# Optimization experiments

Hardware: AMD Instinct MI355X
Metric: run time of the kernel (lower is better)

The kernel has to match this reference:

```python
import jax, jax.numpy as jnp
import numpy as np

B, S, E, H = 2, 2048, 768, 12
DK = E // H


def setup_inputs() -> dict:
    key = jax.random.key(0)
    ks = jax.random.split(key, 8)
    scale = 1.0 / np.sqrt(E)
    return {
        "key": jax.random.normal(ks[0], (B, S, E), jnp.float32),
        "query": jax.random.normal(ks[1], (B, S, E), jnp.float32),
        "value": jax.random.normal(ks[2], (B, S, E), jnp.float32),
        "mask": jax.random.randint(ks[3], (1, 1, S, S), 0, 2, jnp.int32),
        # nn.Linear params (w_k used for q/k/v as in the source; w_o output proj)
        "Wk": jax.random.uniform(ks[4], (E, E), jnp.float32, -scale, scale),
        "bk": jax.random.uniform(ks[5], (E,), jnp.float32, -scale, scale),
        "Wo": jax.random.uniform(ks[6], (E, E), jnp.float32, -scale, scale),
        "bo": jax.random.uniform(ks[7], (E,), jnp.float32, -scale, scale),
    }


def reference(key, query, value, mask, Wk, bk, Wo, bo):
    # NOTE: source module (faithfully) projects q, k, v all with w_k.
    k = (key @ Wk.T + bk).reshape(B, S, H, DK).transpose(0, 2, 1, 3)    # [B,H,S,DK]
    q = (query @ Wk.T + bk).reshape(B, S, H, DK).transpose(0, 2, 1, 3)
    v = (value @ Wk.T + bk).reshape(B, S, H, DK).transpose(0, 2, 1, 3)
    # quirk: scores MULTIPLIED by sqrt(d_k) (source bug, preserved)
    scores = jnp.einsum("bhsd,bhtd->bhst", q, k) * jnp.sqrt(jnp.float32(DK))
    # quirk: masked positions set to 1e-6 (not -inf), BEFORE softmax
    scores = jnp.where(mask == 0, jnp.float32(1e-6), scores)
    # dropout=0.0 -> identity (applied pre-softmax in source)
    attn = jax.nn.softmax(scores, axis=-1)                               # [B,H,S,S]
    x = jnp.einsum("bhst,bhtd->bhsd", attn, v)                           # [B,H,S,DK]
    x = x.transpose(0, 2, 1, 3).reshape(B, S, E)
    return x @ Wo.T + bo
```

## Files before the change

kernel.cpp:

```cpp
#include <hip/hip_runtime.h>

#define BB 2
#define SS 2048
#define EE 768
#define HH 12
#define DKK 64

typedef _Float16 h16;
typedef _Float16 half8 __attribute__((ext_vector_type(8)));
typedef _Float16 h16x4 __attribute__((ext_vector_type(4)));
typedef __fp16 pk2 __attribute__((ext_vector_type(2)));
typedef float f32x4 __attribute__((ext_vector_type(4)));

#define K2F 11.5416173f

__device__ __forceinline__ void gl_lds16(const void* g, void* l) {
    __builtin_amdgcn_global_load_lds(
        (const __attribute__((address_space(1))) unsigned int*)g,
        (__attribute__((address_space(3))) unsigned int*)l, 16, 0, 0);
}

__global__ void cvtpack_k(const float* __restrict__ sK, const float* __restrict__ sQ,
                          const float* __restrict__ sV, const float* __restrict__ sWk,
                          const float* __restrict__ sWo,
                          h16* __restrict__ dK, h16* __restrict__ dQ, h16* __restrict__ dV,
                          h16* __restrict__ dWk, h16* __restrict__ dWo,
                          const int* __restrict__ mask, unsigned* __restrict__ mp) {
    if (blockIdx.x >= 5184) {
        int idx = (blockIdx.x - 5184) * 256 + threadIdx.x;
        int base = idx * 32;
        const int4* m4 = (const int4*)(mask + base);
        unsigned w = 0;
#pragma unroll
        for (int i = 0; i < 8; ++i) {
            int4 v = m4[i];
            if (v.x) w |= 1u << (i * 4 + 0);
            if (v.y) w |= 1u << (i * 4 + 1);
            if (v.z) w |= 1u << (i * 4 + 2);
            if (v.w) w |= 1u << (i * 4 + 3);
        }
        mp[idx] = w;
        return;
    }
    long g = (long)blockIdx.x * 256 + threadIdx.x;
    const float* src;
    h16* dst;
    long off;
    if (g < 393216)        { src = sK;  dst = dK;  off = g; }
    else if (g < 786432)   { src = sQ;  dst = dQ;  off = g - 393216; }
    else if (g < 1179648)  { src = sV;  dst = dV;  off = g - 786432; }
    else if (g < 1253376)  { src = sWk; dst = dWk; off = g - 1179648; }
    else                   { src = sWo; dst = dWo; off = g - 1253376; }
    const float* p = src + off * 8;
    float4 a = *(const float4*)p, b = *(const float4*)(p + 4);
    half8 h = {(h16)a.x, (h16)a.y, (h16)a.z, (h16)a.w,
               (h16)b.x, (h16)b.y, (h16)b.z, (h16)b.w};
    *(half8*)(dst + off * 8) = h;
}

__launch_bounds__(256)
__global__ void proj_gemm_k(const h16* __restrict__ keyh, const h16* __restrict__ qryh,
                            const h16* __restrict__ valh, const h16* __restrict__ Wkh,
                            const float* __restrict__ bk,
                            h16* __restrict__ kh, h16* __restrict__ qh, h16* __restrict__ vtp) {
    __shared__ h16 As[64 * 64];
    __shared__ h16 Bs[128 * 64];
    const int bid = blockIdx.x;
    const int idx = (bid & 7) * 144 + (bid >> 3);
    const int z = idx / 384;
    const int rem = idx % 384;
    const int m0 = (rem / 6) * 64, n0 = (rem % 6) * 128;
    const h16* src = (z == 0) ? keyh : ((z == 1) ? qryh : valh);
    const int tid = threadIdx.x, lane = tid & 63, wid = tid >> 6;
    const int l = lane & 15, gq = lane >> 4;
    f32x4 acc[4][2] = {};

    for (int k0 = 0; k0 < EE; k0 += 64) {
#pragma unroll
        for (int it = 0; it < 2; ++it) {
            int e = it * 256 + tid;
            int row = e >> 3, slot = e & 7;
            gl_lds16(src + (long)(m0 + row) * EE + k0 + ((slot ^ (row & 7)) << 3), As + e * 8);
        }
#pragma unroll
        for (int it = 0; it < 4; ++it) {
            int e = it * 256 + tid;
            int row = e >> 3, slot = e & 7;
            gl_lds16(Wkh + (long)(n0 + row) * EE + k0 + ((slot ^ (row & 7)) << 3), Bs + e * 8);
        }
        __syncthreads();
#pragma unroll
        for (int ks = 0; ks < 2; ++ks) {
            half8 a[4], b[2];
#pragma unroll
            for (int rf = 0; rf < 4; ++rf) {
                int row = rf * 16 + l;
                int g = (ks * 4 + gq) ^ (row & 7);
                a[rf] = *(const half8*)((const char*)As + row * 128 + (g << 4));
            }
#pragma unroll
            for (int cf = 0; cf < 2; ++cf) {
                int row = wid * 32 + cf * 16 + l;
                int g = (ks * 4 + gq) ^ (row & 7);
                b[cf] = *(const half8*)((const char*)Bs + row * 128 + (g << 4));
            }
            __builtin_amdgcn_s_setprio(1);
#pragma unroll
            for (int rf = 0; rf < 4; ++rf)
#pragma unroll
                for (int cf = 0; cf < 2; ++cf)
                    acc[rf][cf] = __builtin_amdgcn_mfma_f32_16x16x32_f16(a[rf], b[cf], acc[rf][cf], 0, 0, 0);
            __builtin_amdgcn_s_setprio(0);
        }
        __syncthreads();
    }
    if (z == 2) {
#pragma unroll
        for (int rf = 0; rf < 4; ++rf)
#pragma unroll
            for (int cf = 0; cf < 2; ++cf) {
                int n = n0 + wid * 32 + cf * 16 + l;
                float bias = bk[n];
                int h = n >> 6, d = n & 63;
                int mb = m0 + rf * 16 + gq * 4;
                int b = mb >> 11, s = mb & 2047;
                h16x4 pv = {(h16)(acc[rf][cf][0] + bias), (h16)(acc[rf][cf][1] + bias),
                            (h16)(acc[rf][cf][2] + bias), (h16)(acc[rf][cf][3] + bias)};
                *(h16x4*)(vtp + ((long)((b * HH + h) * 64 + d)) * SS + s) = pv;
            }
    } else {
        h16* dst = (z == 0) ? kh : qh;
        const float qs = (z == 1) ? K2F : 1.0f;
#pragma unroll
        for (int rf = 0; rf < 4; ++rf)
#pragma unroll
            for (int cf = 0; cf < 2; ++cf) {
                int n = n0 + wid * 32 + cf * 16 + l;
                float bias = bk[n];
                int h = n >> 6, d = n & 63;
#pragma unroll
                for (int j = 0; j < 4; ++j) {
                    int m = m0 + rf * 16 + gq * 4 + j;
                    int b = m >> 11, s = m & 2047;
                    dst[(((long)(b * HH + h) * SS + s) << 6) + d] = (h16)((acc[rf][cf][j] + bias) * qs);
                }
            }
    }
}

#define SMX_GROUP(S, MW, M2, LS, PB)                                               \
  {                                                                                \
    unsigned long long mw = (MW);                                                  \
    unsigned w0 = (unsigned)mw, w1 = (unsigned)(mw >> 32);                         \
    _Pragma("unroll")                                                              \
    for (int cf = 0; cf < 4; ++cf) {                                               \
      unsigned wcb = (cf & 2) ? w1 : w0;                                           \
      _Pragma("unroll")                                                            \
      for (int j = 0; j < 4; ++j) {                                                \
        unsigned sh = ((cf & 1) << 4) + g * 4 + j;                                 \
        S[cf][j] = ((wcb >> sh) & 1u) ? S[cf][j] : C2;                             \
      }                                                                            \
    }                                                                              \
    float pmax = fmaxf(fmaxf(S[0][0], S[0][1]), fmaxf(S[0][2], S[0][3]));          \
    _Pragma("unroll")                                                              \
    for (int cf = 1; cf < 4; ++cf)                                                 \
      pmax = fmaxf(pmax, fmaxf(fmaxf(S[cf][0], S[cf][1]), fmaxf(S[cf][2], S[cf][3]))); \
    if (!__all(pmax <= (M2) + 11.0f)) {                                            \
      pmax = fmaxf(pmax, __shfl_xor(pmax, 16));                                    \
      pmax = fmaxf(pmax, __shfl_xor(pmax, 32));                                    \
      float mnew = fmaxf((M2), pmax);                                              \
      float alpha = __builtin_amdgcn_exp2f((M2) - mnew);                           \
      _Pragma("unroll")                                                            \
      for (int df = 0; df < 4; ++df)                                               \
        _Pragma("unroll")                                                          \
        for (int j = 0; j < 4; ++j) o##PB[df][j] *= alpha;                         \
      (LS) *= alpha;                                                               \
      (M2) = mnew;                                                                 \
    }                                                                              \
    const float negm2 = -(M2);                                                     \
    float rs = 0.f;                                                                \
    _Pragma("unroll")                                                              \
    for (int cf = 0; cf < 4; ++cf)                                                 \
      _Pragma("unroll")                                                            \
      for (int j = 0; j < 4; ++j) {                                                \
        float p = __builtin_amdgcn_exp2f(S[cf][j] + negm2);                        \
        S[cf][j] = p;                                                              \
        rs += p;                                                                   \
      }                                                                            \
    (LS) += rs;                                                                    \
    _Pragma("unroll")                                                              \
    for (int cf = 0; cf < 4; ++cf) {                                               \
      union { pk2 h[2]; unsigned long long u; } pu;                                \
      pu.h[0] = __builtin_amdgcn_cvt_pkrtz(S[cf][0], S[cf][1]);                    \
      pu.h[1] = __builtin_amdgcn_cvt_pkrtz(S[cf][2], S[cf][3]);                    \
      *(unsigned long long*)(pb##PB + pst[cf]) = pu.u;                             \
    }                                                                              \
  }

#define ATTN_TILE(KL, VL, KN, VN, T)                                               \
  {                                                                                \
    long nko = (long)((((T) + 1) & 15)) * (64 * DKK);                              \
    int nvo = (((T) + 1) & 15) * 64;                                               \
    gl_lds16(kgl0 + nko, (KN) + stg0);                                             \
    gl_lds16(kgl1 + nko, (KN) + stg1);                                             \
    gl_lds16(vgl0 + nvo, (VN) + stg0);                                             \
    gl_lds16(vgl1 + nvo, (VN) + stg1);                                             \
    half8 ka[4], kb[4];                                                            \
    _Pragma("unroll")                                                              \
    for (int cf = 0; cf < 4; ++cf) {                                               \
      ka[cf] = *(const half8*)((const char*)(KL) + off0 + cf * 2048);              \
      kb[cf] = *(const half8*)((const char*)(KL) + off1 + cf * 2048);              \
    }                                                                              \
    f32x4 sA[4], sB[4];                                                            \
    __builtin_amdgcn_s_setprio(1);                                                 \
    _Pragma("unroll")                                                              \
    for (int cf = 0; cf < 4; ++cf) {                                               \
      f32x4 z = {};                                                                \
      z = __builtin_amdgcn_mfma_f32_16x16x32_f16(ka[cf], qfA0, z, 0, 0, 0);        \
      z = __builtin_amdgcn_mfma_f32_16x16x32_f16(kb[cf], qfA1, z, 0, 0, 0);        \
      sA[cf] = z;                                                                  \
    }                                                                              \
    _Pragma("unroll")                                                              \
    for (int cf = 0; cf < 4; ++cf) {                                               \
      f32x4 z = {};                                                                \
      z = __builtin_amdgcn_mfma_f32_16x16x32_f16(ka[cf], qfB0, z, 0, 0, 0);        \
      z = __builtin_amdgcn_mfma_f32_16x16x32_f16(kb[cf], qfB1, z, 0, 0, 0);        \
      sB[cf] = z;                                                                  \
    }                                                                              \
    __builtin_amdgcn_s_setprio(0);                                                 \
    SMX_GROUP(sA, mrA[T], m2A, lsA, A)                                             \
    SMX_GROUP(sB, mrB[T], m2B, lsB, B)                                             \
    _Pragma("unroll")                                                              \
    for (int ks = 0; ks < 2; ++ks) {                                               \
      int fo = ks ? off1 : off0;                                                   \
      half8 vk[4];                                                                 \
      _Pragma("unroll")                                                            \
      for (int df = 0; df < 4; ++df)                                               \
        vk[df] = *(const half8*)((const char*)(VL) + fo + df * 2048);              \
      half8 pfA = *(const half8*)(pbA + fo);                                       \
      half8 pfB = *(const half8*)(pbB + fo);                                       \
      __builtin_amdgcn_s_setprio(1);                                               \
      _Pragma("unroll")                                                            \
      for (int df = 0; df < 4; ++df)                                               \
        oA[df] = __builtin_amdgcn_mfma_f32_16x16x32_f16(vk[df], pfA, oA[df], 0, 0, 0); \
      _Pragma("unroll")                                                            \
      for (int df = 0; df < 4; ++df)                                               \
        oB[df] = __builtin_amdgcn_mfma_f32_16x16x32_f16(vk[df], pfB, oB[df], 0, 0, 0); \
      __builtin_amdgcn_s_setprio(0);                                               \
    }                                                                              \
    __syncthreads();                                                               \
  }

__launch_bounds__(256, 3)
__global__ void attn_k(const h16* __restrict__ qh, const h16* __restrict__ kh,
                       const h16* __restrict__ vt, const unsigned long long* __restrict__ mp,
                       h16* __restrict__ pO, float* __restrict__ pML) {
    __shared__ h16 K0[4096], K1[4096], V0[4096], V1[4096];
    __shared__ char Ps[16384];
    const int tid = threadIdx.x;
    const int lane = tid & 63, wid = tid >> 6;
    const int l = lane & 15, g = lane >> 4;
    const int bid = blockIdx.x;
    const int idx = (bid & 7) * 96 + (bid >> 3);
    const int bh = idx >> 5;
    const int rem = idx & 31;
    const int qb = rem >> 1, kvh = rem & 1;
    const int q0w = qb * 128 + wid * 32;
    const long base = (long)bh * SS * DKK;
    char* pbA = Ps + wid * 4096;
    char* pbB = pbA + 2048;

    const int off0 = l * 128 + ((g ^ (l & 7)) << 4);
    const int off1 = l * 128 + (((4 + g) ^ (l & 7)) << 4);
    int pst[4];
#pragma unroll
    for (int cf = 0; cf < 4; ++cf)
        pst[cf] = l * 128 + (((2 * cf + (g >> 1)) ^ (l & 7)) << 4) + (g & 1) * 8;
    const int rr = lane >> 3, sg = (lane & 7) ^ (lane >> 3);
    const int stg0 = wid * 1024 + lane * 8, stg1 = wid * 1024 + 512 + lane * 8;
    const int kvbase = kvh * 1024;
    const h16* kgl0 = kh + base + (long)(kvbase + wid * 16 + rr) * DKK + sg * 8;
    const h16* kgl1 = kgl0 + 8 * DKK;
    const h16* vgl0 = vt + base + (long)(wid * 16 + rr) * SS + kvbase + sg * 8;
    const h16* vgl1 = vgl0 + 8 * SS;

    half8 qfA0, qfA1, qfB0, qfB1;
    {
        const h16* qp = qh + base + (long)(q0w + l) * DKK + g * 8;
        qfA0 = *(const half8*)qp;
        qfA1 = *(const half8*)(qp + 32);
        qfB0 = *(const half8*)(qp + 16 * DKK);
        qfB1 = *(const half8*)(qp + 16 * DKK + 32);
    }
    const unsigned long long* mrA = mp + (long)(q0w + l) * (SS / 64) + kvh * 16;
    const unsigned long long* mrB = mrA + 16 * (SS / 64);

    f32x4 oA[4] = {}, oB[4] = {};
    float m2A = -INFINITY, lsA = 0.f, m2B = -INFINITY, lsB = 0.f;
    const float C2 = 1e-6f * 1.44269504f;

    gl_lds16(kgl0, K0 + stg0);
    gl_lds16(kgl1, K0 + stg1);
    gl_lds16(vgl0, V0 + stg0);
    gl_lds16(vgl1, V0 + stg1);
    __syncthreads();

    for (int it = 0; it < 8; ++it) {
        int t = 2 * it;
        ATTN_TILE(K0, V0, K1, V1, t)
        ATTN_TILE(K1, V1, K0, V0, t + 1)
    }

    lsA += __shfl_xor(lsA, 16);
    lsA += __shfl_xor(lsA, 32);
    lsB += __shfl_xor(lsB, 16);
    lsB += __shfl_xor(lsB, 32);
    long prow = ((long)(bh * 2 + kvh) * 2048 + q0w + l);
    h16* pa = pO + (prow << 6) + g * 4;
    h16* pb = pO + ((prow + 16) << 6) + g * 4;
#pragma unroll
    for (int df = 0; df < 4; ++df) {
        h16x4 vA = {(h16)oA[df][0], (h16)oA[df][1], (h16)oA[df][2], (h16)oA[df][3]};
        h16x4 vB = {(h16)oB[df][0], (h16)oB[df][1], (h16)oB[df][2], (h16)oB[df][3]};
        *(h16x4*)(pa + df * 16) = vA;
        *(h16x4*)(pb + df * 16) = vB;
    }
    if (g == 0) {
        float2* mlp = (float2*)(pML + prow * 2);
        *mlp = make_float2(m2A, lsA);
        *(float2*)(pML + (prow + 16) * 2) = make_float2(m2B, lsB);
    }
}

__global__ void combine_k(const h16* __restrict__ pO, const float* __restrict__ pML,
                          h16* __restrict__ xh) {
    int idx = blockIdx.x * 256 + threadIdx.x;
    int d8 = idx & 7;
    int q = (idx >> 3) & 2047;
    int bh = idx >> 14;
    long r0 = (long)(bh * 2) * 2048 + q, r1 = r0 + 2048;
    float2 ml0 = *(const float2*)(pML + r0 * 2);
    float2 ml1 = *(const float2*)(pML + r1 * 2);
    float ms = fmaxf(ml0.x, ml1.x);
    float w0 = __builtin_amdgcn_exp2f(ml0.x - ms);
    float w1 = __builtin_amdgcn_exp2f(ml1.x - ms);
    float inv = 1.0f / (ml0.y * w0 + ml1.y * w1);
    float s0 = w0 * inv, s1 = w1 * inv;
    half8 o0 = *(const half8*)(pO + (r0 << 6) + d8 * 8);
    half8 o1 = *(const half8*)(pO + (r1 << 6) + d8 * 8);
    int b = bh / HH, h = bh % HH;
    half8 r;
#pragma unroll
    for (int i = 0; i < 8; ++i)
        r[i] = (h16)((float)o0[i] * s0 + (float)o1[i] * s1);
    *(half8*)(xh + (long)(b * SS + q) * EE + h * 64 + d8 * 8) = r;
}

__launch_bounds__(256)
__global__ void out_gemm_k(const h16* __restrict__ xh, const h16* __restrict__ Woh,
                           const float* __restrict__ bo, float* __restrict__ out) {
    __shared__ h16 As[64 * 64];
    __shared__ h16 Bs[64 * 64];
    const int bid = blockIdx.x;
    const int idx = (bid & 7) * 96 + (bid >> 3);
    const int m0 = (idx / 12) * 64, n0 = (idx % 12) * 64;
    const int tid = threadIdx.x, lane = tid & 63, wid = tid >> 6;
    const int l = lane & 15, gq = lane >> 4;
    const int wr = wid >> 1, wc = wid & 1;
    f32x4 acc[2][2] = {};

    for (int k0 = 0; k0 < EE; k0 += 64) {
#pragma unroll
        for (int it = 0; it < 2; ++it) {
            int e = it * 256 + tid;
            int row = e >> 3, slot = e & 7;
            int gsl = (slot ^ (row & 7)) << 3;
            gl_lds16(xh + (long)(m0 + row) * EE + k0 + gsl, As + e * 8);
            gl_lds16(Woh + (long)(n0 + row) * EE + k0 + gsl, Bs + e * 8);
        }
        __syncthreads();
#pragma unroll
        for (int ks = 0; ks < 2; ++ks) {
            half8 a[2], b[2];
#pragma unroll
            for (int rf = 0; rf < 2; ++rf) {
                int row = wr * 32 + rf * 16 + l;
                int g = (ks * 4 + gq) ^ (row & 7);
                a[rf] = *(const half8*)((const char*)As + row * 128 + (g << 4));
            }
#pragma unroll
            for (int cf = 0; cf < 2; ++cf) {
                int row = wc * 32 + cf * 16 + l;
                int g = (ks * 4 + gq) ^ (row & 7);
                b[cf] = *(const half8*)((const char*)Bs + row * 128 + (g << 4));
            }
            __builtin_amdgcn_s_setprio(1);
#pragma unroll
            for (int rf = 0; rf < 2; ++rf)
#pragma unroll
                for (int cf = 0; cf < 2; ++cf)
                    acc[rf][cf] = __builtin_amdgcn_mfma_f32_16x16x32_f16(a[rf], b[cf], acc[rf][cf], 0, 0, 0);
            __builtin_amdgcn_s_setprio(0);
        }
        __syncthreads();
    }
#pragma unroll
    for (int rf = 0; rf < 2; ++rf)
#pragma unroll
        for (int cf = 0; cf < 2; ++cf) {
            int n = n0 + wc * 32 + cf * 16 + l;
            float bias = bo[n];
#pragma unroll
            for (int j = 0; j < 4; ++j) {
                int m = m0 + wr * 32 + rf * 16 + gq * 4 + j;
                out[(long)m * EE + n] = acc[rf][cf][j] + bias;
            }
        }
}

extern "C" void kernel_launch(void* const* d_in, const int* in_sizes, int n_in,
                              void* d_out, int out_size, void* d_ws, size_t ws_size,
                              hipStream_t stream) {
    const float* key   = (const float*)d_in[0];
    const float* query = (const float*)d_in[1];
    const float* value = (const float*)d_in[2];
    const int*   mask  = (const int*)d_in[3];
    const float* Wk    = (const float*)d_in[4];
    const float* bk    = (const float*)d_in[5];
    const float* Wo    = (const float*)d_in[6];
    const float* bo    = (const float*)d_in[7];

    char* ws = (char*)d_ws;
    h16* keyh = (h16*)(ws + 0);
    h16* qryh = (h16*)(ws + 6291456);
    h16* valh = (h16*)(ws + 12582912);
    h16* qh   = (h16*)(ws + 18874368);
    h16* kh   = (h16*)(ws + 25165824);
    h16* vt   = (h16*)(ws + 31457280);
    h16* Wkh  = (h16*)(ws + 37748736);
    h16* Woh  = (h16*)(ws + 38928384);
    unsigned* mp = (unsigned*)(ws + 40108032);
    h16*  pO  = (h16*)(ws + 0);
    float* pML = (float*)(ws + 12582912);
    h16*  xh  = (h16*)(ws + 18874368);
    float* out = (float*)d_out;

    hipLaunchKernelGGL(cvtpack_k, dim3(5696), dim3(256), 0, stream,
                       key, query, value, Wk, Wo, keyh, qryh, valh, Wkh, Woh, mask, mp);
    hipLaunchKernelGGL(proj_gemm_k, dim3(1152), dim3(256), 0, stream,
                       keyh, qryh, valh, Wkh, bk, kh, qh, vt);
    hipLaunchKernelGGL(attn_k, dim3(768), dim3(256), 0, stream,
                       qh, kh, vt, (const unsigned long long*)mp, pO, pML);
    hipLaunchKernelGGL(combine_k, dim3(1536), dim3(256), 0, stream, pO, pML, xh);
    hipLaunchKernelGGL(out_gemm_k, dim3(768), dim3(256), 0, stream, xh, Woh, bo, out);
}
```

Before: 115.9 us.

## Split attention KV range three ways and halve P scratch for higher occupancy

```diff
diff --git a/kernel.cpp b/kernel.cpp
--- a/kernel.cpp
+++ b/kernel.cpp
@@ -148,7 +148,7 @@
     }
 }
 
-#define SMX_GROUP(S, MW, M2, LS, PB)                                               \
+#define SMX_GROUP(S, MW, M2, LS, OACC)                                             \
   {                                                                                \
     unsigned long long mw = (MW);                                                  \
     unsigned w0 = (unsigned)mw, w1 = (unsigned)(mw >> 32);                         \
@@ -173,7 +173,7 @@
       _Pragma("unroll")                                                            \
       for (int df = 0; df < 4; ++df)                                               \
         _Pragma("unroll")                                                          \
-        for (int j = 0; j < 4; ++j) o##PB[df][j] *= alpha;                         \
+        for (int j = 0; j < 4; ++j) OACC[df][j] *= alpha;                          \
       (LS) *= alpha;                                                               \
       (M2) = mnew;                                                                 \
     }                                                                              \
@@ -193,14 +193,34 @@
       union { pk2 h[2]; unsigned long long u; } pu;                                \
       pu.h[0] = __builtin_amdgcn_cvt_pkrtz(S[cf][0], S[cf][1]);                    \
       pu.h[1] = __builtin_amdgcn_cvt_pkrtz(S[cf][2], S[cf][3]);                    \
-      *(unsigned long long*)(pb##PB + pst[cf]) = pu.u;                             \
+      *(unsigned long long*)(pb + pst[cf]) = pu.u;                                 \
+    }                                                                              \
+  }
+
+#define PV_GROUP(VL, OACC)                                                         \
+  {                                                                                \
+    _Pragma("unroll")                                                              \
+    for (int ks = 0; ks < 2; ++ks) {                                               \
+      int fo = ks ? off1 : off0;                                                   \
+      half8 pf = *(const half8*)(pb + fo);                                         \
+      half8 vk[4];                                                                 \
+      _Pragma("unroll")                                                            \
+      for (int df = 0; df < 4; ++df)                                               \
+        vk[df] = *(const half8*)((const char*)(VL) + fo + df * 2048);              \
+      __builtin_amdgcn_s_setprio(1);                                               \
+      _Pragma("unroll")                                                            \
+      for (int df = 0; df < 4; ++df)                                               \
+        OACC[df] = __builtin_amdgcn_mfma_f32_16x16x32_f16(vk[df], pf, OACC[df], 0, 0, 0); \
+      __builtin_amdgcn_s_setprio(0);                                               \
     }                                                                              \
   }
 
 #define ATTN_TILE(KL, VL, KN, VN, T)                                               \
   {                                                                                \
-    long nko = (long)((((T) + 1) & 15)) * (64 * DKK);                              \
-    int nvo = (((T) + 1) & 15) * 64;                                               \
+    int tn = (T) + 1;                                                              \
+    if (tn == nt) tn = 0;                                                          \
+    long nko = (long)tn * (64 * DKK);                                              \
+    int nvo = tn * 64;                                                             \
     gl_lds16(kgl0 + nko, (KN) + stg0);                                             \
     gl_lds16(kgl1 + nko, (KN) + stg1);                                             \
     gl_lds16(vgl0 + nvo, (VN) + stg0);                                             \
@@ -228,47 +248,32 @@
       sB[cf] = z;                                                                  \
     }                                                                              \
     __builtin_amdgcn_s_setprio(0);                                                 \
-    SMX_GROUP(sA, mrA[T], m2A, lsA, A)                                             \
-    SMX_GROUP(sB, mrB[T], m2B, lsB, B)                                             \
-    _Pragma("unroll")                                                              \
-    for (int ks = 0; ks < 2; ++ks) {                                               \
-      int fo = ks ? off1 : off0;                                                   \
-      half8 vk[4];                                                                 \
-      _Pragma("unroll")                                                            \
-      for (int df = 0; df < 4; ++df)                                               \
-        vk[df] = *(const half8*)((const char*)(VL) + fo + df * 2048);              \
-      half8 pfA = *(const half8*)(pbA + fo);                                       \
-      half8 pfB = *(const half8*)(pbB + fo);                                       \
-      __builtin_amdgcn_s_setprio(1);                                               \
-      _Pragma("unroll")                                                            \
-      for (int df = 0; df < 4; ++df)                                               \
-        oA[df] = __builtin_amdgcn_mfma_f32_16x16x32_f16(vk[df], pfA, oA[df], 0, 0, 0); \
-      _Pragma("unroll")                                                            \
-      for (int df = 0; df < 4; ++df)                                               \
-        oB[df] = __builtin_amdgcn_mfma_f32_16x16x32_f16(vk[df], pfB, oB[df], 0, 0, 0); \
-      __builtin_amdgcn_s_setprio(0);                                               \
-    }                                                                              \
+    SMX_GROUP(sA, mrA[T], m2A, lsA, oA)                                            \
+    PV_GROUP(VL, oA)                                                               \
+    SMX_GROUP(sB, mrB[T], m2B, lsB, oB)                                            \
+    PV_GROUP(VL, oB)                                                               \
     __syncthreads();                                                               \
   }
 
-__launch_bounds__(256, 3)
+__launch_bounds__(256, 4)
 __global__ void attn_k(const h16* __restrict__ qh, const h16* __restrict__ kh,
                        const h16* __restrict__ vt, const unsigned long long* __restrict__ mp,
                        h16* __restrict__ pO, float* __restrict__ pML) {
     __shared__ h16 K0[4096], K1[4096], V0[4096], V1[4096];
-    __shared__ char Ps[16384];
+    __shared__ char Ps[8192];
     const int tid = threadIdx.x;
     const int lane = tid & 63, wid = tid >> 6;
     const int l = lane & 15, g = lane >> 4;
     const int bid = blockIdx.x;
-    const int idx = (bid & 7) * 96 + (bid >> 3);
-    const int bh = idx >> 5;
-    const int rem = idx & 31;
-    const int qb = rem >> 1, kvh = rem & 1;
+    const int idx = (bid & 7) * 144 + (bid >> 3);
+    const int bh = idx / 48;
+    const int rem = idx % 48;
+    const int qb = rem / 3, kvh = rem % 3;
+    const int nt = (kvh == 2) ? 10 : 11;
+    const int kvt0 = kvh * 11;
     const int q0w = qb * 128 + wid * 32;
     const long base = (long)bh * SS * DKK;
-    char* pbA = Ps + wid * 4096;
-    char* pbB = pbA + 2048;
+    char* pb = Ps + wid * 2048;
 
     const int off0 = l * 128 + ((g ^ (l & 7)) << 4);
     const int off1 = l * 128 + (((4 + g) ^ (l & 7)) << 4);
@@ -278,10 +283,9 @@
         pst[cf] = l * 128 + (((2 * cf + (g >> 1)) ^ (l & 7)) << 4) + (g & 1) * 8;
     const int rr = lane >> 3, sg = (lane & 7) ^ (lane >> 3);
     const int stg0 = wid * 1024 + lane * 8, stg1 = wid * 1024 + 512 + lane * 8;
-    const int kvbase = kvh * 1024;
-    const h16* kgl0 = kh + base + (long)(kvbase + wid * 16 + rr) * DKK + sg * 8;
+    const h16* kgl0 = kh + base + (long)(kvt0 * 64 + wid * 16 + rr) * DKK + sg * 8;
     const h16* kgl1 = kgl0 + 8 * DKK;
-    const h16* vgl0 = vt + base + (long)(wid * 16 + rr) * SS + kvbase + sg * 8;
+    const h16* vgl0 = vt + base + (long)(wid * 16 + rr) * SS + kvt0 * 64 + sg * 8;
     const h16* vgl1 = vgl0 + 8 * SS;
 
     half8 qfA0, qfA1, qfB0, qfB1;
@@ -292,7 +296,7 @@
         qfB0 = *(const half8*)(qp + 16 * DKK);
         qfB1 = *(const half8*)(qp + 16 * DKK + 32);
     }
-    const unsigned long long* mrA = mp + (long)(q0w + l) * (SS / 64) + kvh * 16;
+    const unsigned long long* mrA = mp + (long)(q0w + l) * (SS / 64) + kvt0;
     const unsigned long long* mrB = mrA + 16 * (SS / 64);
 
     f32x4 oA[4] = {}, oB[4] = {};
@@ -305,29 +309,32 @@
     gl_lds16(vgl1, V0 + stg1);
     __syncthreads();
 
-    for (int it = 0; it < 8; ++it) {
+    for (int it = 0; it < (nt >> 1); ++it) {
         int t = 2 * it;
         ATTN_TILE(K0, V0, K1, V1, t)
         ATTN_TILE(K1, V1, K0, V0, t + 1)
+    }
+    if (nt & 1) {
+        int t = nt - 1;
+        ATTN_TILE(K0, V0, K1, V1, t)
     }
 
     lsA += __shfl_xor(lsA, 16);
     lsA += __shfl_xor(lsA, 32);
     lsB += __shfl_xor(lsB, 16);
     lsB += __shfl_xor(lsB, 32);
-    long prow = ((long)(bh * 2 + kvh) * 2048 + q0w + l);
+    long prow = ((long)(bh * 3 + kvh) * 2048 + q0w + l);
     h16* pa = pO + (prow << 6) + g * 4;
-    h16* pb = pO + ((prow + 16) << 6) + g * 4;
+    h16* pbo = pO + ((prow + 16) << 6) + g * 4;
 #pragma unroll
     for (int df = 0; df < 4; ++df) {
         h16x4 vA = {(h16)oA[df][0], (h16)oA[df][1], (h16)oA[df][2], (h16)oA[df][3]};
         h16x4 vB = {(h16)oB[df][0], (h16)oB[df][1], (h16)oB[df][2], (h16)oB[df][3]};
         *(h16x4*)(pa + df * 16) = vA;
-        *(h16x4*)(pb + df * 16) = vB;
+        *(h16x4*)(pbo + df * 16) = vB;
     }
     if (g == 0) {
-        float2* mlp = (float2*)(pML + prow * 2);
-        *mlp = make_float2(m2A, lsA);
+        *(float2*)(pML + prow * 2) = make_float2(m2A, lsA);
         *(float2*)(pML + (prow + 16) * 2) = make_float2(m2B, lsB);
     }
 }
@@ -338,21 +345,24 @@
     int d8 = idx & 7;
     int q = (idx >> 3) & 2047;
     int bh = idx >> 14;
-    long r0 = (long)(bh * 2) * 2048 + q, r1 = r0 + 2048;
+    long r0 = (long)(bh * 3) * 2048 + q, r1 = r0 + 2048, r2 = r0 + 4096;
     float2 ml0 = *(const float2*)(pML + r0 * 2);
     float2 ml1 = *(const float2*)(pML + r1 * 2);
-    float ms = fmaxf(ml0.x, ml1.x);
+    float2 ml2 = *(const float2*)(pML + r2 * 2);
+    float ms = fmaxf(fmaxf(ml0.x, ml1.x), ml2.x);
     float w0 = __builtin_amdgcn_exp2f(ml0.x - ms);
     float w1 = __builtin_amdgcn_exp2f(ml1.x - ms);
-    float inv = 1.0f / (ml0.y * w0 + ml1.y * w1);
-    float s0 = w0 * inv, s1 = w1 * inv;
+    float w2 = __builtin_amdgcn_exp2f(ml2.x - ms);
+    float inv = 1.0f / (ml0.y * w0 + ml1.y * w1 + ml2.y * w2);
+    float s0 = w0 * inv, s1 = w1 * inv, s2 = w2 * inv;
     half8 o0 = *(const half8*)(pO + (r0 << 6) + d8 * 8);
     half8 o1 = *(const half8*)(pO + (r1 << 6) + d8 * 8);
+    half8 o2 = *(const half8*)(pO + (r2 << 6) + d8 * 8);
     int b = bh / HH, h = bh % HH;
     half8 r;
 #pragma unroll
     for (int i = 0; i < 8; ++i)
-        r[i] = (h16)((float)o0[i] * s0 + (float)o1[i] * s1);
+        r[i] = (h16)((float)o0[i] * s0 + (float)o1[i] * s1 + (float)o2[i] * s2);
     *(half8*)(xh + (long)(b * SS + q) * EE + h * 64 + d8 * 8) = r;
 }
 
@@ -441,7 +451,7 @@
     h16* Woh  = (h16*)(ws + 38928384);
     unsigned* mp = (unsigned*)(ws + 40108032);
     h16*  pO  = (h16*)(ws + 0);
-    float* pML = (float*)(ws + 12582912);
+    float* pML = (float*)d_out;
     h16*  xh  = (h16*)(ws + 18874368);
     float* out = (float*)d_out;
 
@@ -449,7 +459,7 @@
                        key, query, value, Wk, Wo, keyh, qryh, valh, Wkh, Woh, mask, mp);
     hipLaunchKernelGGL(proj_gemm_k, dim3(1152), dim3(256), 0, stream,
                        keyh, qryh, valh, Wkh, bk, kh, qh, vt);
-    hipLaunchKernelGGL(attn_k, dim3(768), dim3(256), 0, stream,
+    hipLaunchKernelGGL(attn_k, dim3(1152), dim3(256), 0, stream,
                        qh, kh, vt, (const unsigned long long*)mp, pO, pML);
     hipLaunchKernelGGL(combine_k, dim3(1536), dim3(256), 0, stream, pO, pML, xh);
     hipLaunchKernelGGL(out_gemm_k, dim3(768), dim3(256), 0, stream, xh, Woh, bo, out);
```

New measurement: 167.4 us. +44.4%, slower.
